# Optimization experiments

Hardware: AMD Instinct MI355X
Metric: run time of the kernel (lower is better)

Reference implementation:

```python
import jax, jax.numpy as jnp
import numpy as np

TEMPERATURE = 1.0
NEG = -1e9
EPS = 1e-8


def setup_inputs() -> dict:
    key = jax.random.key(0)
    k1, k2, k3 = jax.random.split(key, 3)
    B, H = 524288, 32
    scores = jax.random.normal(k1, (B, H), dtype=jnp.float32)
    rankings = jax.random.randint(k2, (B, H), 0, 33, dtype=jnp.int32)
    mask = jax.random.randint(k3, (B, H), 0, 2, dtype=jnp.int32).astype(bool)
    return {"scores": scores, "rankings": rankings, "mask": mask}


def reference(scores, rankings, mask):
    B, H = scores.shape
    # effective validity: horse present AND has a ranking > 0 (top_k=None)
    m = mask & (rankings > 0)
    # masked, temperature-scaled scores; -1e9 entries underflow to exactly 0 in softmax
    s = jnp.where(m, scores / TEMPERATURE, NEG)
    p = jax.nn.softmax(s, axis=1)  # [B, H], ~0 at invalid slots

    n_valid = jnp.sum(m, axis=1)  # [B]
    # ideal order: valid horses sorted by ranking ascending (invalid pushed to end)
    rank_key = jnp.where(m, rankings, jnp.iinfo(jnp.int32).max)
    rank_order = jnp.argsort(rank_key, axis=1)          # stable sort
    # prediction order: valid horses in original index order (matches torch.where)
    pos_order = jnp.argsort(~m, axis=1)                 # stable: valid first

    q = jnp.take_along_axis(p, rank_order, axis=1)      # ideal_probs, aligned by list position
    pr = jnp.take_along_axis(p, pos_order, axis=1)      # pred_probs,  aligned by list position

    # positions >= n_valid are padding
    valid_pos = jnp.arange(H)[None, :] < n_valid[:, None]
    q_safe = jnp.where(valid_pos, q, 1.0)
    pr_safe = jnp.where(valid_pos, pr, 1.0)
    # KL(ideal || pred) with the original's log(pred + 1e-8)
    kl_terms = q_safe * (jnp.log(q_safe) - jnp.log(pr_safe + EPS))
    kl = jnp.sum(jnp.where(valid_pos, kl_terms, 0.0), axis=1)  # [B]

    # rows with <= 1 valid ranked horse are skipped entirely
    row_ok = n_valid > 1
    n_rows = jnp.maximum(jnp.sum(row_ok), 1)
    return jnp.sum(jnp.where(row_ok, kl, 0.0)) / n_rows  # reduction='mean'
```

## Files before the change

kernel.cpp:

```cpp
#include <hip/hip_runtime.h>
#include <stdint.h>


#define H 32
#define BLK 256
#define WPB 4
#define WROW 33
#define WREGION (64 * WROW)

typedef short s16x2 __attribute__((ext_vector_type(2)));
union PK { uint32_t u; s16x2 v; };

__global__ __launch_bounds__(BLK) void listwise_kernel(
    const float* __restrict__ scores,
    const int* __restrict__ rankings,
    const unsigned char* __restrict__ mask_u8,
    float* __restrict__ part_kl,
    float* __restrict__ part_cnt,
    int nrows)
{
    __shared__ uint32_t stage[WPB * WREGION];
    __shared__ float s_kl[WPB], s_cnt[WPB];

    const int tid  = threadIdx.x;
    const int lane = tid & 63;
    const int wid  = tid >> 6;
    uint32_t* wbuf = &stage[wid * WREGION];
    const int wrow0 = blockIdx.x * BLK + wid * 64;

    unsigned char probe = mask_u8[lane];
    const bool mask_is_i32 =
        (__ballot(((lane & 3) != 0) && (probe != 0)) == 0ull);

    float kl = 0.0f, cnt = 0.0f;

    uint32_t kp[16], sp[16], vbits = 0;
    int nv = 0;
    bool have_row = false;
    unsigned short* rowp = (unsigned short*)&wbuf[lane * WROW];

    if (wrow0 + 64 <= nrows) {
        have_row = true;
        if (mask_is_i32) {
            const uint4* g4 =
                (const uint4*)((const uint32_t*)mask_u8 + (size_t)wrow0 * H);
            #pragma unroll
            for (int c = 0; c < 8; ++c) {
                uint4 v = g4[lane + 64 * c];
                const int L = (lane + 64 * c) << 2;
                uint32_t* d = &wbuf[(L >> 5) * WROW + (L & 31)];
                d[0] = v.x; d[1] = v.y; d[2] = v.z; d[3] = v.w;
            }
            const uint32_t* rb = &wbuf[lane * WROW];
            #pragma unroll
            for (int k = 0; k < H; ++k)
                vbits |= (rb[k] != 0u ? 1u : 0u) << k;
        } else {
            const uint4* g4 = (const uint4*)(mask_u8 + (size_t)wrow0 * H);
            #pragma unroll
            for (int c = 0; c < 2; ++c) {
                uint4 v = g4[lane + 64 * c];
                const int L = (lane + 64 * c) << 2;
                uint32_t* d = &wbuf[(L >> 3) * 9 + (L & 7)];
                d[0] = v.x; d[1] = v.y; d[2] = v.z; d[3] = v.w;
            }
            const uint32_t* rb = &wbuf[lane * 9];
            #pragma unroll
            for (int dwi = 0; dwi < 8; ++dwi) {
                uint32_t w = rb[dwi];
                uint32_t t2 = w | (w >> 1); t2 |= t2 >> 2; t2 |= t2 >> 4;
                uint32_t nib = ((t2 & 0x01010101u) * 0x01020408u) >> 24;
                vbits |= (nib & 0xFu) << (dwi * 4);
            }
        }

        {
            const uint4* g4 = (const uint4*)(rankings + (size_t)wrow0 * H);
            #pragma unroll
            for (int c = 0; c < 8; ++c) {
                uint4 v = g4[lane + 64 * c];
                const int L = (lane + 64 * c) << 2;
                uint32_t* d = &wbuf[(L >> 5) * WROW + (L & 31)];
                d[0] = v.x; d[1] = v.y; d[2] = v.z; d[3] = v.w;
            }
            const int* rb = (const int*)&wbuf[lane * WROW];
            #pragma unroll
            for (int a = 0; a < 16; ++a) {
                const int r0 = rb[2 * a], r1 = rb[2 * a + 1];
                const bool v0 = (((vbits >> (2 * a)) & 1u) != 0u) && (r0 > 0);
                const bool v1 = (((vbits >> (2 * a + 1)) & 1u) != 0u) && (r1 > 0);
                const uint32_t k0 = v0 ? ((((uint32_t)r0) << 5) | (uint32_t)(2 * a))
                                       : (0x4000u | (uint32_t)(2 * a));
                const uint32_t k1 = v1 ? ((((uint32_t)r1) << 5) | (uint32_t)(2 * a + 1))
                                       : (0x4000u | (uint32_t)(2 * a + 1));
                kp[a] = k0 | (k1 << 16);
                nv += (v0 ? 1 : 0) + (v1 ? 1 : 0);
            }
        }

        {
            const uint4* g4 = (const uint4*)(scores + (size_t)wrow0 * H);
            #pragma unroll
            for (int c = 0; c < 8; ++c) {
                uint4 v = g4[lane + 64 * c];
                const int L = (lane + 64 * c) << 2;
                uint32_t* d = &wbuf[(L >> 5) * WROW + (L & 31)];
                d[0] = v.x; d[1] = v.y; d[2] = v.z; d[3] = v.w;
            }
            const uint32_t* rb = &wbuf[lane * WROW];
            int jp = 0;
            #pragma unroll
            for (int a = 0; a < 16; ++a) {
                const uint32_t b0 = (rb[2 * a]     + 0x8000u) >> 16;
                const uint32_t b1 = (rb[2 * a + 1] + 0x8000u) >> 16;
                sp[a] = b0 | (b1 << 16);
                const uint32_t kw = kp[a];
                const bool v0 = (kw & 0xFFFFu) < 0x4000u;
                const bool v1 = (kw >> 16) < 0x4000u;
                rowp[v0 ? jp : 64] = (unsigned short)b0;
                jp += v0 ? 1 : 0;
                rowp[v1 ? jp : 64] = (unsigned short)b1;
                jp += v1 ? 1 : 0;
            }
        }
    } else if (wrow0 + lane < nrows) {
        have_row = true;
        const int row = wrow0 + lane;
        const int*   rptr = rankings + (size_t)row * H;
        const float* sptr = scores + (size_t)row * H;
        if (mask_is_i32) {
            const int* mp = (const int*)mask_u8 + (size_t)row * H;
            #pragma unroll
            for (int k = 0; k < H; ++k) vbits |= (mp[k] != 0 ? 1u : 0u) << k;
        } else {
            const unsigned char* mp = mask_u8 + (size_t)row * H;
            #pragma unroll
            for (int k = 0; k < H; ++k) vbits |= (mp[k] != 0 ? 1u : 0u) << k;
        }
        int jp = 0;
        #pragma unroll
        for (int a = 0; a < 16; ++a) {
            uint32_t kq[2], bq[2];
            #pragma unroll
            for (int q = 0; q < 2; ++q) {
                const int k = 2 * a + q;
                const int r = rptr[k];
                const bool valid = (((vbits >> k) & 1u) != 0u) && (r > 0);
                kq[q] = valid ? ((((uint32_t)r) << 5) | (uint32_t)k)
                              : (0x4000u | (uint32_t)k);
                nv += valid ? 1 : 0;
                bq[q] = (__float_as_uint(sptr[k]) + 0x8000u) >> 16;
                rowp[valid ? jp : 64] = (unsigned short)bq[q];
                jp += valid ? 1 : 0;
            }
            kp[a] = kq[0] | (kq[1] << 16);
            sp[a] = bq[0] | (bq[1] << 16);
        }
    }

    if (have_row) {
        float se = 0.0f, num = 0.0f;
        #pragma unroll
        for (int i = 0; i < H; ++i) {
            const uint32_t pw = kp[i / 2];
            const uint32_t k16 = (i & 1) ? (pw >> 16) : (pw & 0xFFFFu);
            PK b; b.u = (k16 << 16) | k16;
            PK acc; acc.u = 0;
            #pragma unroll
            for (int m = 0; m < 16; ++m) {
                PK pm; pm.u = kp[m];
                s16x2 d = pm.v - b.v;
                acc.v = acc.v - (d >> 15);
            }
            const int j = (int)acc.v.x + (int)acc.v.y;
            const float g = __uint_as_float(((uint32_t)rowp[j]) << 16);
            const uint32_t sw = sp[i / 2];
            const float s_i = __uint_as_float((i & 1) ? (sw & 0xFFFF0000u)
                                                      : (sw << 16));
            const bool valid = k16 < 0x4000u;
            float e = __expf(s_i);
            e = valid ? e : 0.0f;
            const float d2 = valid ? (s_i - g) : 0.0f;
            se += e;
            num = __builtin_fmaf(e, d2, num);
        }
        if (nv > 1) { kl = __fdividef(num, se); cnt = 1.0f; }
    }

    #pragma unroll
    for (int m = 32; m >= 1; m >>= 1) {
        kl  += __shfl_xor(kl, m);
        cnt += __shfl_xor(cnt, m);
    }
    if (lane == 0) { s_kl[wid] = kl; s_cnt[wid] = cnt; }
    __syncthreads();
    if (tid == 0) {
        part_kl[blockIdx.x]  = s_kl[0] + s_kl[1] + s_kl[2] + s_kl[3];
        part_cnt[blockIdx.x] = s_cnt[0] + s_cnt[1] + s_cnt[2] + s_cnt[3];
    }
}

__global__ __launch_bounds__(256) void finalize_kernel(
    const float* __restrict__ part_kl,
    const float* __restrict__ part_cnt,
    float* __restrict__ out, int nblk)
{
    float k = 0.0f, c = 0.0f;
    for (int i = threadIdx.x; i < nblk; i += 256) {
        k += part_kl[i];
        c += part_cnt[i];
    }
    #pragma unroll
    for (int m = 32; m >= 1; m >>= 1) {
        k += __shfl_xor(k, m);
        c += __shfl_xor(c, m);
    }
    __shared__ float sk[4], sc[4];
    const int wid = threadIdx.x >> 6;
    if ((threadIdx.x & 63) == 0) { sk[wid] = k; sc[wid] = c; }
    __syncthreads();
    if (threadIdx.x == 0) {
        float K = sk[0] + sk[1] + sk[2] + sk[3];
        float C = sc[0] + sc[1] + sc[2] + sc[3];
        if (C < 1.0f) C = 1.0f;
        out[0] = K / C;
    }
}

extern "C" void kernel_launch(void* const* d_in, const int* in_sizes, int n_in,
                              void* d_out, int out_size, void* d_ws, size_t ws_size,
                              hipStream_t stream) {
    const float* scores = (const float*)d_in[0];
    const int* rankings = (const int*)d_in[1];
    const unsigned char* mask = (const unsigned char*)d_in[2];
    float* out = (float*)d_out;

    const int total = in_sizes[0];
    const int nrows = total / H;
    const int blocks = (nrows + BLK - 1) / BLK;

    float* part_kl  = (float*)d_ws;
    float* part_cnt = (float*)d_ws + blocks;

    listwise_kernel<<<blocks, BLK, 0, stream>>>(
        scores, rankings, mask, part_kl, part_cnt, nrows);

    finalize_kernel<<<1, 256, 0, stream>>>(part_kl, part_cnt, out, blocks);
}
```

Measured before the change: 207.1 us.

## Pack keys and bf16 scores before LDS staging, halving shared-memory footprint

Rankings and mask are loaded together and combined into packed 16-bit sort keys in registers before the shared-memory transpose. Scores are converted to bf16 and packed two per word before staging. This halves the per-row LDS stride (33 to 17 words), removes separate staging passes and the vbits construction, and derives the valid count from packed flag bits. The cost is more register work at load time, and the smaller LDS buffer could change occupancy.

Result: no change. 207.2 us (+0.0%).

```diff
diff --git a/kernel.cpp b/kernel.cpp
--- a/kernel.cpp
+++ b/kernel.cpp
@@ -5,8 +5,8 @@
 #define H 32
 #define BLK 256
 #define WPB 4
-#define WROW 33
-#define WREGION (64 * WROW)
+#define ROWD 17
+#define WREGION (64 * ROWD)
 
 typedef short s16x2 __attribute__((ext_vector_type(2)));
 union PK { uint32_t u; s16x2 v; };
@@ -34,92 +34,85 @@
 
     float kl = 0.0f, cnt = 0.0f;
 
-    uint32_t kp[16], sp[16], vbits = 0;
+    uint32_t kp[16], sp[16];
     int nv = 0;
     bool have_row = false;
-    unsigned short* rowp = (unsigned short*)&wbuf[lane * WROW];
+    unsigned short* rowp = (unsigned short*)&wbuf[lane * ROWD];
 
     if (wrow0 + 64 <= nrows) {
         have_row = true;
+
+        const uint4* r4 = (const uint4*)(rankings + (size_t)wrow0 * H);
         if (mask_is_i32) {
-            const uint4* g4 =
+            const uint4* m4 =
                 (const uint4*)((const uint32_t*)mask_u8 + (size_t)wrow0 * H);
             #pragma unroll
             for (int c = 0; c < 8; ++c) {
-                uint4 v = g4[lane + 64 * c];
+                const uint4 rv = r4[lane + 64 * c];
+                const uint4 mv = m4[lane + 64 * c];
                 const int L = (lane + 64 * c) << 2;
-                uint32_t* d = &wbuf[(L >> 5) * WROW + (L & 31)];
-                d[0] = v.x; d[1] = v.y; d[2] = v.z; d[3] = v.w;
-            }
-            const uint32_t* rb = &wbuf[lane * WROW];
-            #pragma unroll
-            for (int k = 0; k < H; ++k)
-                vbits |= (rb[k] != 0u ? 1u : 0u) << k;
+                const uint32_t t0 = (mv.x != 0u && (int)rv.x > 0) ? (rv.x << 5) : 0x4000u;
+                const uint32_t t1 = (mv.y != 0u && (int)rv.y > 0) ? (rv.y << 5) : 0x4000u;
+                const uint32_t t2 = (mv.z != 0u && (int)rv.z > 0) ? (rv.z << 5) : 0x4000u;
+                const uint32_t t3 = (mv.w != 0u && (int)rv.w > 0) ? (rv.w << 5) : 0x4000u;
+                uint32_t* d = &wbuf[(L >> 5) * ROWD + ((L & 31) >> 1)];
+                d[0] = t0 | (t1 << 16);
+                d[1] = t2 | (t3 << 16);
+            }
         } else {
-            const uint4* g4 = (const uint4*)(mask_u8 + (size_t)wrow0 * H);
-            #pragma unroll
-            for (int c = 0; c < 2; ++c) {
-                uint4 v = g4[lane + 64 * c];
+            const uint32_t* m1 = (const uint32_t*)(mask_u8 + (size_t)wrow0 * H);
+            #pragma unroll
+            for (int c = 0; c < 8; ++c) {
+                const uint4 rv = r4[lane + 64 * c];
+                const uint32_t mv = m1[lane + 64 * c];
                 const int L = (lane + 64 * c) << 2;
-                uint32_t* d = &wbuf[(L >> 3) * 9 + (L & 7)];
-                d[0] = v.x; d[1] = v.y; d[2] = v.z; d[3] = v.w;
-            }
-            const uint32_t* rb = &wbuf[lane * 9];
-            #pragma unroll
-            for (int dwi = 0; dwi < 8; ++dwi) {
-                uint32_t w = rb[dwi];
-                uint32_t t2 = w | (w >> 1); t2 |= t2 >> 2; t2 |= t2 >> 4;
-                uint32_t nib = ((t2 & 0x01010101u) * 0x01020408u) >> 24;
-                vbits |= (nib & 0xFu) << (dwi * 4);
-            }
-        }
-
+                const uint32_t t0 = ((mv & 0x000000FFu) != 0u && (int)rv.x > 0) ? (rv.x << 5) : 0x4000u;
+                const uint32_t t1 = ((mv & 0x0000FF00u) != 0u && (int)rv.y > 0) ? (rv.y << 5) : 0x4000u;
+                const uint32_t t2 = ((mv & 0x00FF0000u) != 0u && (int)rv.z > 0) ? (rv.z << 5) : 0x4000u;
+                const uint32_t t3 = ((mv & 0xFF000000u) != 0u && (int)rv.w > 0) ? (rv.w << 5) : 0x4000u;
+                uint32_t* d = &wbuf[(L >> 5) * ROWD + ((L & 31) >> 1)];
+                d[0] = t0 | (t1 << 16);
+                d[1] = t2 | (t3 << 16);
+            }
+        }
         {
-            const uint4* g4 = (const uint4*)(rankings + (size_t)wrow0 * H);
-            #pragma unroll
-            for (int c = 0; c < 8; ++c) {
-                uint4 v = g4[lane + 64 * c];
-                const int L = (lane + 64 * c) << 2;
-                uint32_t* d = &wbuf[(L >> 5) * WROW + (L & 31)];
-                d[0] = v.x; d[1] = v.y; d[2] = v.z; d[3] = v.w;
-            }
-            const int* rb = (const int*)&wbuf[lane * WROW];
+            const uint32_t* rb = &wbuf[lane * ROWD];
+            uint32_t inv2 = 0;
             #pragma unroll
             for (int a = 0; a < 16; ++a) {
-                const int r0 = rb[2 * a], r1 = rb[2 * a + 1];
-                const bool v0 = (((vbits >> (2 * a)) & 1u) != 0u) && (r0 > 0);
-                const bool v1 = (((vbits >> (2 * a + 1)) & 1u) != 0u) && (r1 > 0);
-                const uint32_t k0 = v0 ? ((((uint32_t)r0) << 5) | (uint32_t)(2 * a))
-                                       : (0x4000u | (uint32_t)(2 * a));
-                const uint32_t k1 = v1 ? ((((uint32_t)r1) << 5) | (uint32_t)(2 * a + 1))
-                                       : (0x4000u | (uint32_t)(2 * a + 1));
-                kp[a] = k0 | (k1 << 16);
-                nv += (v0 ? 1 : 0) + (v1 ? 1 : 0);
-            }
+                const uint32_t w = rb[a];
+                kp[a] = w | ((uint32_t)(2 * a) | (((uint32_t)(2 * a + 1)) << 16));
+                inv2 += (w >> 14) & 0x00010001u;
+            }
+            nv = 32 - (int)((inv2 & 0xFFFFu) + (inv2 >> 16));
         }
 
         {
             const uint4* g4 = (const uint4*)(scores + (size_t)wrow0 * H);
             #pragma unroll
             for (int c = 0; c < 8; ++c) {
-                uint4 v = g4[lane + 64 * c];
+                const uint4 v = g4[lane + 64 * c];
                 const int L = (lane + 64 * c) << 2;
-                uint32_t* d = &wbuf[(L >> 5) * WROW + (L & 31)];
-                d[0] = v.x; d[1] = v.y; d[2] = v.z; d[3] = v.w;
-            }
-            const uint32_t* rb = &wbuf[lane * WROW];
+                const uint32_t b0 = (v.x + 0x8000u) >> 16;
+                const uint32_t b1 = (v.y + 0x8000u) >> 16;
+                const uint32_t b2 = (v.z + 0x8000u) >> 16;
+                const uint32_t b3 = (v.w + 0x8000u) >> 16;
+                uint32_t* d = &wbuf[(L >> 5) * ROWD + ((L & 31) >> 1)];
+                d[0] = b0 | (b1 << 16);
+                d[1] = b2 | (b3 << 16);
+            }
+            const uint32_t* rb = &wbuf[lane * ROWD];
             int jp = 0;
             #pragma unroll
             for (int a = 0; a < 16; ++a) {
-                const uint32_t b0 = (rb[2 * a]     + 0x8000u) >> 16;
-                const uint32_t b1 = (rb[2 * a + 1] + 0x8000u) >> 16;
-                sp[a] = b0 | (b1 << 16);
+                const uint32_t sw = rb[a];
+                sp[a] = sw;
                 const uint32_t kw = kp[a];
                 const bool v0 = (kw & 0xFFFFu) < 0x4000u;
                 const bool v1 = (kw >> 16) < 0x4000u;
-                rowp[v0 ? jp : 64] = (unsigned short)b0;
+                rowp[v0 ? jp : 33] = (unsigned short)(sw & 0xFFFFu);
                 jp += v0 ? 1 : 0;
-                rowp[v1 ? jp : 64] = (unsigned short)b1;
+                rowp[v1 ? jp : 33] = (unsigned short)(sw >> 16);
                 jp += v1 ? 1 : 0;
             }
         }
@@ -128,6 +121,7 @@
         const int row = wrow0 + lane;
         const int*   rptr = rankings + (size_t)row * H;
         const float* sptr = scores + (size_t)row * H;
+        uint32_t vbits = 0;
         if (mask_is_i32) {
             const int* mp = (const int*)mask_u8 + (size_t)row * H;
             #pragma unroll
@@ -150,7 +144,7 @@
                               : (0x4000u | (uint32_t)k);
                 nv += valid ? 1 : 0;
                 bq[q] = (__float_as_uint(sptr[k]) + 0x8000u) >> 16;
-                rowp[valid ? jp : 64] = (unsigned short)bq[q];
+                rowp[valid ? jp : 33] = (unsigned short)bq[q];
                 jp += valid ? 1 : 0;
             }
             kp[a] = kq[0] | (kq[1] << 16);
```
